# Kernel tuning notes

Hardware: AMD Instinct MI355X
Metric: run time of the kernel (lower is better)

Reference implementation:

```python
import jax, jax.numpy as jnp
import numpy as np

EPS = 1e-13

def masked_softmax(scores, mask):
    # scores: [B, Lq, Lk], mask: [B, Lk] (float 0/1)
    # ESIM masked_softmax: softmax(scores * mask), zero masked cols, renormalize.
    m = mask[:, None, :]
    p = jax.nn.softmax(scores * m, axis=-1)
    p = p * m
    return p / (jnp.sum(p, axis=-1, keepdims=True) + EPS)

def weighted_sum(tensor, weights, mask):
    # tensor: [B, Lk, D], weights: [B, Lq, Lk], mask: [B, Lq]
    ws = jnp.einsum('bqk,bkd->bqd', weights, tensor)
    return ws * mask[:, :, None]

def setup_inputs() -> dict:
    key = jax.random.key(0)
    B, Lp, Lh, D, Dg = 32, 192, 192, 1024, 1024
    ks = jax.random.split(key, 6)
    premise_batch = jax.random.normal(ks[0], (B, Lp, D), jnp.float32)
    hypothesis_batch = jax.random.normal(ks[1], (B, Lh, D), jnp.float32)
    encoded_graph_emb_p = jax.random.normal(ks[2], (B, Lp, Dg), jnp.float32)
    encoded_graph_emb_h = jax.random.normal(ks[3], (B, Lh, Dg), jnp.float32)
    # realistic padding masks: prefix of ones up to a random length
    lp = jax.random.randint(ks[4], (B,), Lp // 2, Lp + 1)
    lh = jax.random.randint(ks[5], (B,), Lh // 2, Lh + 1)
    premise_mask = (jnp.arange(Lp)[None, :] < lp[:, None]).astype(jnp.float32)
    hypothesis_mask = (jnp.arange(Lh)[None, :] < lh[:, None]).astype(jnp.float32)
    return {
        'premise_batch': premise_batch,
        'premise_mask': premise_mask,
        'hypothesis_batch': hypothesis_batch,
        'hypothesis_mask': hypothesis_mask,
        'encoded_graph_emb_p': encoded_graph_emb_p,
        'encoded_graph_emb_h': encoded_graph_emb_h,
    }

def reference(premise_batch, premise_mask, hypothesis_batch, hypothesis_mask,
              encoded_graph_emb_p, encoded_graph_emb_h):
    # [B, Lp, Lh]
    similarity_matrix = jnp.einsum('bpd,bhd->bph', premise_batch, hypothesis_batch)
    similarity_matrix_g = jnp.einsum('bpd,bhd->bph', encoded_graph_emb_p, encoded_graph_emb_h)

    prem_hyp_attn = masked_softmax(similarity_matrix, hypothesis_mask)
    hyp_prem_attn = masked_softmax(jnp.swapaxes(similarity_matrix, 1, 2), premise_mask)
    prem_hyp_attn_g = masked_softmax(similarity_matrix_g, hypothesis_mask)
    hyp_prem_attn_g = masked_softmax(jnp.swapaxes(similarity_matrix_g, 1, 2), premise_mask)

    tot_attn_p = prem_hyp_attn + prem_hyp_attn_g
    tot_attn_h = hyp_prem_attn + hyp_prem_attn_g

    attended_premises = weighted_sum(hypothesis_batch, tot_attn_p, premise_mask)
    attended_hypotheses = weighted_sum(premise_batch, tot_attn_h, hypothesis_mask)
    attended_premises_g = weighted_sum(encoded_graph_emb_h, prem_hyp_attn_g, premise_mask)
    attended_hypotheses_g = weighted_sum(encoded_graph_emb_p, hyp_prem_attn_g, hypothesis_mask)

    return (tot_attn_p, tot_attn_h, attended_premises, attended_premises_g,
            attended_hypotheses, attended_hypotheses_g, prem_hyp_attn,
            hyp_prem_attn, prem_hyp_attn_g, hyp_prem_attn_g)
```

## Files before the change

### kernel.cpp

```cpp
#include <hip/hip_runtime.h>

constexpr int Bb = 32;
constexpr int L  = 192;
constexpr int Dk = 1024;
constexpr size_t A1 = (size_t)Bb * L * L;
constexpr size_t C1 = (size_t)Bb * L * Dk;

typedef short bf16x8 __attribute__((ext_vector_type(8)));
typedef float f32x4  __attribute__((ext_vector_type(4)));
typedef unsigned short ushort_t;

__device__ __forceinline__ unsigned short f2bf(float x){
  unsigned u = __float_as_uint(x);
  u = (u + 0x7FFFu + ((u >> 16) & 1u)) >> 16;
  return (unsigned short)u;
}
__device__ __forceinline__ float bf2f(unsigned short h){
  return __uint_as_float(((unsigned)h) << 16);
}
__device__ __forceinline__ bf16x8 ldfrag(const unsigned short* p){
  return *reinterpret_cast<const bf16x8*>(p);
}

__global__ __launch_bounds__(256) void sim_kernel(
    const float* __restrict__ P, const float* __restrict__ H,
    const float* __restrict__ Gp, const float* __restrict__ Gh,
    float* __restrict__ Sp, float* __restrict__ Sgp)
{
  const int orig = blockIdx.x;
  const int wg   = (orig & 7) * (2304 / 8) + (orig >> 3);
  const int tile = wg % 9;
  const int g    = wg / 9;
  const int ch   = g & 3;
  const int m    = (g >> 2) & 1;
  const int b    = g >> 3;

  const float* X = m ? Gp : P;
  const float* Y = m ? Gh : H;
  float* O = (m ? Sgp : Sp) + (size_t)ch * A1;

  const int ty = tile / 3, tx = tile % 3;
  const int brow = ty * 64, bcol = tx * 64;

  __shared__ unsigned short Ah[64][72], Al[64][72], Bh[64][72], Bl[64][72];

  const int tid  = threadIdx.x;
  const int r    = tid >> 2, q = tid & 3;
  const int lane = tid & 63, wid = tid >> 6;
  const int wm   = wid >> 1, wn = wid & 1;
  const int lr   = lane & 15, kg = lane >> 4;

  f32x4 acc[2][2] = {};

  const float* Xbase = X + (size_t)(b * L + brow + r) * Dk;
  const float* Ybase = Y + (size_t)(b * L + bcol + r) * Dk;
  const int k0beg = ch * 256;

  float4 xv[4], yv[4];

  auto load_regs = [&](int k0){
    #pragma unroll
    for (int j = 0; j < 4; ++j){
      const int c = (q + 4 * j) * 4;
      xv[j] = *reinterpret_cast<const float4*>(Xbase + k0 + c);
      yv[j] = *reinterpret_cast<const float4*>(Ybase + k0 + c);
    }
  };
  auto convert_store = [&](){
    #pragma unroll
    for (int j = 0; j < 4; ++j){
      const int c = (q + 4 * j) * 4;
      ushort4 hh, ll;
      hh.x = f2bf(xv[j].x); ll.x = f2bf(xv[j].x - bf2f(hh.x));
      hh.y = f2bf(xv[j].y); ll.y = f2bf(xv[j].y - bf2f(hh.y));
      hh.z = f2bf(xv[j].z); ll.z = f2bf(xv[j].z - bf2f(hh.z));
      hh.w = f2bf(xv[j].w); ll.w = f2bf(xv[j].w - bf2f(hh.w));
      *reinterpret_cast<ushort4*>(&Ah[r][c]) = hh;
      *reinterpret_cast<ushort4*>(&Al[r][c]) = ll;
      hh.x = f2bf(yv[j].x); ll.x = f2bf(yv[j].x - bf2f(hh.x));
      hh.y = f2bf(yv[j].y); ll.y = f2bf(yv[j].y - bf2f(hh.y));
      hh.z = f2bf(yv[j].z); ll.z = f2bf(yv[j].z - bf2f(hh.z));
      hh.w = f2bf(yv[j].w); ll.w = f2bf(yv[j].w - bf2f(hh.w));
      *reinterpret_cast<ushort4*>(&Bh[r][c]) = hh;
      *reinterpret_cast<ushort4*>(&Bl[r][c]) = ll;
    }
  };

  load_regs(k0beg);
  convert_store();
  __syncthreads();

  for (int chunk = 0; chunk < 4; ++chunk){
    if (chunk < 3) load_regs(k0beg + (chunk + 1) * 64);

    #pragma unroll
    for (int kk = 0; kk < 64; kk += 32){
      const int ki = kk + kg * 8;
      bf16x8 ah[2], al[2], bh[2], bl[2];
      ah[0] = ldfrag(&Ah[wm * 32 +      lr][ki]);
      ah[1] = ldfrag(&Ah[wm * 32 + 16 + lr][ki]);
      al[0] = ldfrag(&Al[wm * 32 +      lr][ki]);
      al[1] = ldfrag(&Al[wm * 32 + 16 + lr][ki]);
      bh[0] = ldfrag(&Bh[wn * 32 +      lr][ki]);
      bh[1] = ldfrag(&Bh[wn * 32 + 16 + lr][ki]);
      bl[0] = ldfrag(&Bl[wn * 32 +      lr][ki]);
      bl[1] = ldfrag(&Bl[wn * 32 + 16 + lr][ki]);
      #pragma unroll
      for (int tm = 0; tm < 2; ++tm)
        #pragma unroll
        for (int tn = 0; tn < 2; ++tn){
          acc[tm][tn] = __builtin_amdgcn_mfma_f32_16x16x32_bf16(ah[tm], bh[tn], acc[tm][tn], 0, 0, 0);
          acc[tm][tn] = __builtin_amdgcn_mfma_f32_16x16x32_bf16(ah[tm], bl[tn], acc[tm][tn], 0, 0, 0);
          acc[tm][tn] = __builtin_amdgcn_mfma_f32_16x16x32_bf16(al[tm], bh[tn], acc[tm][tn], 0, 0, 0);
        }
    }
    __syncthreads();
    if (chunk < 3){
      convert_store();
      __syncthreads();
    }
  }

  float* Ob = O + (size_t)b * L * L;
  #pragma unroll
  for (int tm = 0; tm < 2; ++tm)
    #pragma unroll
    for (int tn = 0; tn < 2; ++tn){
      const int row0 = brow + wm * 32 + tm * 16 + kg * 4;
      const int col  = bcol + wn * 32 + tn * 16 + lr;
      #pragma unroll
      for (int i = 0; i < 4; ++i)
        Ob[(size_t)(row0 + i) * L + col] = acc[tm][tn][i];
    }
}

__global__ __launch_bounds__(256) void row_softmax(
    const float* __restrict__ Sp, const float* __restrict__ Sgp,
    const float* __restrict__ hmask,
    float* __restrict__ o7, float* __restrict__ o9, float* __restrict__ o1,
    float* __restrict__ Sred, float* __restrict__ Sgred,
    ushort_t* __restrict__ w1, ushort_t* __restrict__ w9)
{
  const int b    = blockIdx.y;
  const int p    = blockIdx.x * 4 + (threadIdx.x >> 6);
  const int lane = threadIdx.x & 63;
  const size_t rowoff = ((size_t)b * L + p) * L;
  const float* sr  = Sp  + rowoff;
  const float* sgr = Sgp + rowoff;
  const float* mk  = hmask + (size_t)b * L;

  float m[3], raw[3], rawg[3], v[3], vg[3];
  #pragma unroll
  for (int j = 0; j < 3; ++j){
    const int h = lane + 64 * j;
    const float mm = mk[h];
    m[j]    = mm;
    raw[j]  = sr [h] + sr [A1 + h] + sr [2*A1 + h] + sr [3*A1 + h];
    rawg[j] = sgr[h] + sgr[A1 + h] + sgr[2*A1 + h] + sgr[3*A1 + h];
    v[j]  = raw[j]  * mm;
    vg[j] = rawg[j] * mm;
    Sred [rowoff + h] = raw[j];
    Sgred[rowoff + h] = rawg[j];
  }
  float M  = fmaxf(fmaxf(v[0],  v[1]),  v[2]);
  float Mg = fmaxf(fmaxf(vg[0], vg[1]), vg[2]);
  #pragma unroll
  for (int off = 32; off; off >>= 1){
    M  = fmaxf(M,  __shfl_xor(M,  off));
    Mg = fmaxf(Mg, __shfl_xor(Mg, off));
  }
  float e[3], eg[3];
  float Z = 0.f, Zg = 0.f, Ein = 0.f, Eing = 0.f;
  #pragma unroll
  for (int j = 0; j < 3; ++j){
    e[j]  = expf(v[j]  - M);
    eg[j] = expf(vg[j] - Mg);
    Z  += e[j];  Ein  += m[j] * e[j];
    Zg += eg[j]; Eing += m[j] * eg[j];
  }
  #pragma unroll
  for (int off = 32; off; off >>= 1){
    Z    += __shfl_xor(Z,    off);
    Zg   += __shfl_xor(Zg,   off);
    Ein  += __shfl_xor(Ein,  off);
    Eing += __shfl_xor(Eing, off);
  }
  const float inv  = 1.f / (Ein  + 1e-13f * Z);
  const float invg = 1.f / (Eing + 1e-13f * Zg);
  #pragma unroll
  for (int j = 0; j < 3; ++j){
    const int h = lane + 64 * j;
    const float rj  = m[j] * e[j]  * inv;
    const float rgj = m[j] * eg[j] * invg;
    o7[rowoff + h] = rj;
    o9[rowoff + h] = rgj;
    o1[rowoff + h] = rj + rgj;
    if (w1){
      w1[rowoff + h] = f2bf(rj + rgj);
      w9[rowoff + h] = f2bf(rgj);
    }
  }
}

__global__ __launch_bounds__(256) void col_softmax(
    const float* __restrict__ Sred, const float* __restrict__ Sgred,
    const float* __restrict__ pmask,
    float* __restrict__ o8, float* __restrict__ o10, float* __restrict__ o2,
    ushort_t* __restrict__ w2, ushort_t* __restrict__ w10)
{
  __shared__ float Ts[192][33], Tg[192][33];
  const int b  = blockIdx.y;
  const int h0 = blockIdx.x * 32;
  const int tid = threadIdx.x;
  const size_t boff = (size_t)b * L * L;

  for (int i = tid; i < 192 * 8; i += 256){
    const int rr = i >> 3, qq = i & 7;
    const size_t base = boff + (size_t)rr * L + h0 + qq * 4;
    float4 a = *reinterpret_cast<const float4*>(&Sred[base]);
    float4 g = *reinterpret_cast<const float4*>(&Sgred[base]);
    Ts[rr][qq*4+0] = a.x; Ts[rr][qq*4+1] = a.y; Ts[rr][qq*4+2] = a.z; Ts[rr][qq*4+3] = a.w;
    Tg[rr][qq*4+0] = g.x; Tg[rr][qq*4+1] = g.y; Tg[rr][qq*4+2] = g.z; Tg[rr][qq*4+3] = g.w;
  }
  __syncthreads();

  const int lane = tid & 63, wid = tid >> 6;
  const float* mk = pmask + (size_t)b * L;
  float m[3];
  #pragma unroll
  for (int j = 0; j < 3; ++j) m[j] = mk[lane + 64 * j];

  for (int c = 0; c < 8; ++c){
    const int hl = wid * 8 + c;
    const int h  = h0 + hl;
    float v[3], vg[3];
    #pragma unroll
    for (int j = 0; j < 3; ++j){
      v[j]  = Ts[lane + 64 * j][hl] * m[j];
      vg[j] = Tg[lane + 64 * j][hl] * m[j];
    }
    float M  = fmaxf(fmaxf(v[0],  v[1]),  v[2]);
    float Mg = fmaxf(fmaxf(vg[0], vg[1]), vg[2]);
    #pragma unroll
    for (int off = 32; off; off >>= 1){
      M  = fmaxf(M,  __shfl_xor(M,  off));
      Mg = fmaxf(Mg, __shfl_xor(Mg, off));
    }
    float e[3], eg[3];
    float Z = 0.f, Zg = 0.f, Ein = 0.f, Eing = 0.f;
    #pragma unroll
    for (int j = 0; j < 3; ++j){
      e[j]  = expf(v[j]  - M);
      eg[j] = expf(vg[j] - Mg);
      Z  += e[j];  Ein  += m[j] * e[j];
      Zg += eg[j]; Eing += m[j] * eg[j];
    }
    #pragma unroll
    for (int off = 32; off; off >>= 1){
      Z    += __shfl_xor(Z,    off);
      Zg   += __shfl_xor(Zg,   off);
      Ein  += __shfl_xor(Ein,  off);
      Eing += __shfl_xor(Eing, off);
    }
    const float inv  = 1.f / (Ein  + 1e-13f * Z);
    const float invg = 1.f / (Eing + 1e-13f * Zg);
    const size_t rowoff = ((size_t)b * L + h) * L;
    #pragma unroll
    for (int j = 0; j < 3; ++j){
      const int pp = lane + 64 * j;
      const float rj  = m[j] * e[j]  * inv;
      const float rgj = m[j] * eg[j] * invg;
      o8 [rowoff + pp] = rj;
      o10[rowoff + pp] = rgj;
      o2 [rowoff + pp] = rj + rgj;
      if (w2){
        w2 [rowoff + pp] = f2bf(rj + rgj);
        w10[rowoff + pp] = f2bf(rgj);
      }
    }
  }
}

__global__ __launch_bounds__(256) void wsum_kernel(
    const float* __restrict__ o1f, const float* __restrict__ o9f,
    const float* __restrict__ o2f, const float* __restrict__ o10f,
    const ushort_t* __restrict__ w1, const ushort_t* __restrict__ w9,
    const ushort_t* __restrict__ w2, const ushort_t* __restrict__ w10,
    const float* __restrict__ Pb, const float* __restrict__ Hb,
    const float* __restrict__ Gp, const float* __restrict__ Gh,
    const float* __restrict__ pmask, const float* __restrict__ hmask,
    float* __restrict__ o3, float* __restrict__ o4,
    float* __restrict__ o5, float* __restrict__ o6)
{
  const float* Wf; const ushort_t* Wh; const float* V; const float* qm; float* O;
  switch (blockIdx.z){
    case 0:  Wf = o1f;  Wh = w1;  V = Hb; qm = pmask; O = o3; break;
    case 1:  Wf = o9f;  Wh = w9;  V = Gh; qm = pmask; O = o4; break;
    case 2:  Wf = o2f;  Wh = w2;  V = Pb; qm = hmask; O = o5; break;
    default: Wf = o10f; Wh = w10; V = Gp; qm = hmask; O = o6; break;
  }
  const int b  = blockIdx.y;
  const int d0 = blockIdx.x * 64;

  __shared__ unsigned short Vt[64][68];

  const int tid  = threadIdx.x;
  const int r    = tid >> 2, q = tid & 3;
  const int lane = tid & 63, wv = tid >> 6;
  const int lr   = lane & 15, kg = lane >> 4;

  f32x4 acc[3][4] = {};

  for (int ck = 0; ck < 3; ++ck){
    const int k0 = ck * 64;

    bf16x8 afr[3][2];
    if (Wh){
      #pragma unroll
      for (int t = 0; t < 3; ++t)
        #pragma unroll
        for (int s = 0; s < 2; ++s){
          const int row = wv * 48 + t * 16 + lr;
          afr[t][s] = *reinterpret_cast<const bf16x8*>(
              Wh + ((size_t)b * L + row) * L + k0 + s * 32 + kg * 8);
        }
    } else {
      #pragma unroll
      for (int t = 0; t < 3; ++t)
        #pragma unroll
        for (int s = 0; s < 2; ++s){
          const int row = wv * 48 + t * 16 + lr;
          const float* wp = Wf + ((size_t)b * L + row) * L + k0 + s * 32 + kg * 8;
          float4 x0 = *reinterpret_cast<const float4*>(wp);
          float4 x1 = *reinterpret_cast<const float4*>(wp + 4);
          bf16x8 vv;
          vv[0] = f2bf(x0.x); vv[1] = f2bf(x0.y); vv[2] = f2bf(x0.z); vv[3] = f2bf(x0.w);
          vv[4] = f2bf(x1.x); vv[5] = f2bf(x1.y); vv[6] = f2bf(x1.z); vv[7] = f2bf(x1.w);
          afr[t][s] = vv;
        }
    }

    #pragma unroll
    for (int j = 0; j < 4; ++j){
      const int dcol = (q + 4 * j) * 4;
      float4 vvv = *reinterpret_cast<const float4*>(
          V + ((size_t)b * L + k0 + r) * Dk + d0 + dcol);
      Vt[dcol + 0][r] = f2bf(vvv.x);
      Vt[dcol + 1][r] = f2bf(vvv.y);
      Vt[dcol + 2][r] = f2bf(vvv.z);
      Vt[dcol + 3][r] = f2bf(vvv.w);
    }
    __syncthreads();

    #pragma unroll
    for (int s = 0; s < 2; ++s){
      const int ki = s * 32 + kg * 8;
      bf16x8 bfr[4];
      #pragma unroll
      for (int n = 0; n < 4; ++n)
        bfr[n] = ldfrag(&Vt[n * 16 + lr][ki]);
      #pragma unroll
      for (int t = 0; t < 3; ++t)
        #pragma unroll
        for (int n = 0; n < 4; ++n)
          acc[t][n] = __builtin_amdgcn_mfma_f32_16x16x32_bf16(afr[t][s], bfr[n], acc[t][n], 0, 0, 0);
    }
    __syncthreads();
  }

  #pragma unroll
  for (int t = 0; t < 3; ++t){
    const int row0 = wv * 48 + t * 16 + kg * 4;
    #pragma unroll
    for (int i = 0; i < 4; ++i){
      const int row  = row0 + i;
      const float mv = qm[(size_t)b * L + row];
      #pragma unroll
      for (int n = 0; n < 4; ++n)
        O[((size_t)b * L + row) * Dk + d0 + n * 16 + lr] = acc[t][n][i] * mv;
    }
  }
}

extern "C" void kernel_launch(void* const* d_in, const int* in_sizes, int n_in,
                              void* d_out, int out_size, void* d_ws, size_t ws_size,
                              hipStream_t stream) {
  const float* P  = (const float*)d_in[0];
  const float* pm = (const float*)d_in[1];
  const float* H  = (const float*)d_in[2];
  const float* hm = (const float*)d_in[3];
  const float* Gp = (const float*)d_in[4];
  const float* Gh = (const float*)d_in[5];
  float* out = (float*)d_out;

  float* o1  = out;
  float* o2  = out + A1;
  float* o3  = out + 2 * A1;
  float* o4  = o3 + C1;
  float* o5  = o3 + 2 * C1;
  float* o6  = o3 + 3 * C1;
  float* o7  = o3 + 4 * C1;
  float* o8  = o7 + A1;
  float* o9  = o7 + 2 * A1;
  float* o10 = o7 + 3 * A1;

  float* Sp  = o5;
  float* Sgp = o6;
  float* Sred  = o3;
  float* Sgred = o3 + A1;

  ushort_t* wb = (ws_size >= 4 * A1 * sizeof(ushort_t)) ? (ushort_t*)d_ws : nullptr;
  ushort_t* w1  = wb ? wb + 0 * A1 : nullptr;
  ushort_t* w9  = wb ? wb + 1 * A1 : nullptr;
  ushort_t* w2  = wb ? wb + 2 * A1 : nullptr;
  ushort_t* w10 = wb ? wb + 3 * A1 : nullptr;

  sim_kernel <<<dim3(2304), 256, 0, stream>>>(P, H, Gp, Gh, Sp, Sgp);
  row_softmax<<<dim3(48, 32), 256, 0, stream>>>(Sp, Sgp, hm, o7, o9, o1, Sred, Sgred, w1, w9);
  col_softmax<<<dim3(6, 32),  256, 0, stream>>>(Sred, Sgred, pm, o8, o10, o2, w2, w10);
  wsum_kernel<<<dim3(16, 32, 4), 256, 0, stream>>>(o1, o9, o2, o10, w1, w9, w2, w10,
                                                   P, H, Gp, Gh, pm, hm, o3, o4, o5, o6);
}
```

Measured before the change: 105.5 us.

## Halve split-K partials, drop reduced score buffers, truncate bf16 conversions, swizzle wsum grid

The similarity GEMM now splits K into 2 chunks of 512 instead of 4 of 256. This halves the partial-sum traffic and lets row/col softmax read and sum the two partials directly, so the Sred/Sgred intermediate writes go away. The hi/lo bf16 split uses truncation with byte-permute packing instead of round-to-nearest, and V is truncated to bf16 in the weighted-sum kernel. The wsum launch becomes a 1D grid with an XCD-aware swizzle so blocks sharing the same batch stay together. Costs are fewer sim blocks with longer K loops, which may lower parallelism, and slightly lower precision from truncation.

Result: faster. 90.64 us (-14.1%).

```diff
diff --git a/kernel.cpp b/kernel.cpp
--- a/kernel.cpp
+++ b/kernel.cpp
@@ -15,11 +15,11 @@
   u = (u + 0x7FFFu + ((u >> 16) & 1u)) >> 16;
   return (unsigned short)u;
 }
-__device__ __forceinline__ float bf2f(unsigned short h){
-  return __uint_as_float(((unsigned)h) << 16);
-}
 __device__ __forceinline__ bf16x8 ldfrag(const unsigned short* p){
   return *reinterpret_cast<const bf16x8*>(p);
+}
+__device__ __forceinline__ unsigned pack_hi16(unsigned ua, unsigned ub){
+  return __builtin_amdgcn_perm(ua, ub, 0x03020706u);
 }
 
 __global__ __launch_bounds__(256) void sim_kernel(
@@ -28,12 +28,12 @@
     float* __restrict__ Sp, float* __restrict__ Sgp)
 {
   const int orig = blockIdx.x;
-  const int wg   = (orig & 7) * (2304 / 8) + (orig >> 3);
+  const int wg   = (orig & 7) * (1152 / 8) + (orig >> 3);
   const int tile = wg % 9;
   const int g    = wg / 9;
-  const int ch   = g & 3;
-  const int m    = (g >> 2) & 1;
-  const int b    = g >> 3;
+  const int ch   = g & 1;
+  const int m    = (g >> 1) & 1;
+  const int b    = g >> 2;
 
   const float* X = m ? Gp : P;
   const float* Y = m ? Gh : H;
@@ -54,7 +54,7 @@
 
   const float* Xbase = X + (size_t)(b * L + brow + r) * Dk;
   const float* Ybase = Y + (size_t)(b * L + bcol + r) * Dk;
-  const int k0beg = ch * 256;
+  const int k0beg = ch * 512;
 
   float4 xv[4], yv[4];
 
@@ -66,23 +66,29 @@
       yv[j] = *reinterpret_cast<const float4*>(Ybase + k0 + c);
     }
   };
+  auto split_pack = [](const float4& v, uint2& hi, uint2& lo){
+    unsigned ux = __float_as_uint(v.x), uy = __float_as_uint(v.y);
+    unsigned uz = __float_as_uint(v.z), uw = __float_as_uint(v.w);
+    float lx = v.x - __uint_as_float(ux & 0xFFFF0000u);
+    float ly = v.y - __uint_as_float(uy & 0xFFFF0000u);
+    float lz = v.z - __uint_as_float(uz & 0xFFFF0000u);
+    float lw = v.w - __uint_as_float(uw & 0xFFFF0000u);
+    hi.x = pack_hi16(ux, uy);
+    hi.y = pack_hi16(uz, uw);
+    lo.x = pack_hi16(__float_as_uint(lx), __float_as_uint(ly));
+    lo.y = pack_hi16(__float_as_uint(lz), __float_as_uint(lw));
+  };
   auto convert_store = [&](){
     #pragma unroll
     for (int j = 0; j < 4; ++j){
       const int c = (q + 4 * j) * 4;
-      ushort4 hh, ll;
-      hh.x = f2bf(xv[j].x); ll.x = f2bf(xv[j].x - bf2f(hh.x));
-      hh.y = f2bf(xv[j].y); ll.y = f2bf(xv[j].y - bf2f(hh.y));
-      hh.z = f2bf(xv[j].z); ll.z = f2bf(xv[j].z - bf2f(hh.z));
-      hh.w = f2bf(xv[j].w); ll.w = f2bf(xv[j].w - bf2f(hh.w));
-      *reinterpret_cast<ushort4*>(&Ah[r][c]) = hh;
-      *reinterpret_cast<ushort4*>(&Al[r][c]) = ll;
-      hh.x = f2bf(yv[j].x); ll.x = f2bf(yv[j].x - bf2f(hh.x));
-      hh.y = f2bf(yv[j].y); ll.y = f2bf(yv[j].y - bf2f(hh.y));
-      hh.z = f2bf(yv[j].z); ll.z = f2bf(yv[j].z - bf2f(hh.z));
-      hh.w = f2bf(yv[j].w); ll.w = f2bf(yv[j].w - bf2f(hh.w));
-      *reinterpret_cast<ushort4*>(&Bh[r][c]) = hh;
-      *reinterpret_cast<ushort4*>(&Bl[r][c]) = ll;
+      uint2 hi, lo;
+      split_pack(xv[j], hi, lo);
+      *reinterpret_cast<uint2*>(&Ah[r][c]) = hi;
+      *reinterpret_cast<uint2*>(&Al[r][c]) = lo;
+      split_pack(yv[j], hi, lo);
+      *reinterpret_cast<uint2*>(&Bh[r][c]) = hi;
+      *reinterpret_cast<uint2*>(&Bl[r][c]) = lo;
     }
   };
 
@@ -90,8 +96,8 @@
   convert_store();
   __syncthreads();
 
-  for (int chunk = 0; chunk < 4; ++chunk){
-    if (chunk < 3) load_regs(k0beg + (chunk + 1) * 64);
+  for (int chunk = 0; chunk < 8; ++chunk){
+    if (chunk < 7) load_regs(k0beg + (chunk + 1) * 64);
 
     #pragma unroll
     for (int kk = 0; kk < 64; kk += 32){
@@ -115,7 +121,7 @@
         }
     }
     __syncthreads();
-    if (chunk < 3){
+    if (chunk < 7){
       convert_store();
       __syncthreads();
     }
@@ -138,7 +144,6 @@
     const float* __restrict__ Sp, const float* __restrict__ Sgp,
     const float* __restrict__ hmask,
     float* __restrict__ o7, float* __restrict__ o9, float* __restrict__ o1,
-    float* __restrict__ Sred, float* __restrict__ Sgred,
     ushort_t* __restrict__ w1, ushort_t* __restrict__ w9)
 {
   const int b    = blockIdx.y;
@@ -149,18 +154,14 @@
   const float* sgr = Sgp + rowoff;
   const float* mk  = hmask + (size_t)b * L;
 
-  float m[3], raw[3], rawg[3], v[3], vg[3];
+  float m[3], v[3], vg[3];
   #pragma unroll
   for (int j = 0; j < 3; ++j){
     const int h = lane + 64 * j;
     const float mm = mk[h];
-    m[j]    = mm;
-    raw[j]  = sr [h] + sr [A1 + h] + sr [2*A1 + h] + sr [3*A1 + h];
-    rawg[j] = sgr[h] + sgr[A1 + h] + sgr[2*A1 + h] + sgr[3*A1 + h];
-    v[j]  = raw[j]  * mm;
-    vg[j] = rawg[j] * mm;
-    Sred [rowoff + h] = raw[j];
-    Sgred[rowoff + h] = rawg[j];
+    m[j]  = mm;
+    v[j]  = (sr [h] + sr [A1 + h]) * mm;
+    vg[j] = (sgr[h] + sgr[A1 + h]) * mm;
   }
   float M  = fmaxf(fmaxf(v[0],  v[1]),  v[2]);
   float Mg = fmaxf(fmaxf(vg[0], vg[1]), vg[2]);
@@ -203,7 +204,7 @@
 }
 
 __global__ __launch_bounds__(256) void col_softmax(
-    const float* __restrict__ Sred, const float* __restrict__ Sgred,
+    const float* __restrict__ Sp, const float* __restrict__ Sgp,
     const float* __restrict__ pmask,
     float* __restrict__ o8, float* __restrict__ o10, float* __restrict__ o2,
     ushort_t* __restrict__ w2, ushort_t* __restrict__ w10)
@@ -217,8 +218,12 @@
   for (int i = tid; i < 192 * 8; i += 256){
     const int rr = i >> 3, qq = i & 7;
     const size_t base = boff + (size_t)rr * L + h0 + qq * 4;
-    float4 a = *reinterpret_cast<const float4*>(&Sred[base]);
-    float4 g = *reinterpret_cast<const float4*>(&Sgred[base]);
+    float4 a  = *reinterpret_cast<const float4*>(&Sp [base]);
+    float4 a2 = *reinterpret_cast<const float4*>(&Sp [A1 + base]);
+    float4 g  = *reinterpret_cast<const float4*>(&Sgp[base]);
+    float4 g2 = *reinterpret_cast<const float4*>(&Sgp[A1 + base]);
+    a.x += a2.x; a.y += a2.y; a.z += a2.z; a.w += a2.w;
+    g.x += g2.x; g.y += g2.y; g.z += g2.z; g.w += g2.w;
     Ts[rr][qq*4+0] = a.x; Ts[rr][qq*4+1] = a.y; Ts[rr][qq*4+2] = a.z; Ts[rr][qq*4+3] = a.w;
     Tg[rr][qq*4+0] = g.x; Tg[rr][qq*4+1] = g.y; Tg[rr][qq*4+2] = g.z; Tg[rr][qq*4+3] = g.w;
   }
@@ -292,15 +297,21 @@
     float* __restrict__ o3, float* __restrict__ o4,
     float* __restrict__ o5, float* __restrict__ o6)
 {
+  const int orig = blockIdx.x;
+  const int wg   = (orig & 7) * (2048 / 8) + (orig >> 3);
+  const int dt   = wg & 15;
+  const int gz   = wg >> 4;
+  const int z    = gz & 3;
+  const int b    = gz >> 2;
+  const int d0   = dt * 64;
+
   const float* Wf; const ushort_t* Wh; const float* V; const float* qm; float* O;
-  switch (blockIdx.z){
+  switch (z){
     case 0:  Wf = o1f;  Wh = w1;  V = Hb; qm = pmask; O = o3; break;
     case 1:  Wf = o9f;  Wh = w9;  V = Gh; qm = pmask; O = o4; break;
     case 2:  Wf = o2f;  Wh = w2;  V = Pb; qm = hmask; O = o5; break;
     default: Wf = o10f; Wh = w10; V = Gp; qm = hmask; O = o6; break;
   }
-  const int b  = blockIdx.y;
-  const int d0 = blockIdx.x * 64;
 
   __shared__ unsigned short Vt[64][68];
 
@@ -345,10 +356,10 @@
       const int dcol = (q + 4 * j) * 4;
       float4 vvv = *reinterpret_cast<const float4*>(
           V + ((size_t)b * L + k0 + r) * Dk + d0 + dcol);
-      Vt[dcol + 0][r] = f2bf(vvv.x);
-      Vt[dcol + 1][r] = f2bf(vvv.y);
-      Vt[dcol + 2][r] = f2bf(vvv.z);
-      Vt[dcol + 3][r] = f2bf(vvv.w);
+      Vt[dcol + 0][r] = (ushort_t)(__float_as_uint(vvv.x) >> 16);
+      Vt[dcol + 1][r] = (ushort_t)(__float_as_uint(vvv.y) >> 16);
+      Vt[dcol + 2][r] = (ushort_t)(__float_as_uint(vvv.z) >> 16);
+      Vt[dcol + 3][r] = (ushort_t)(__float_as_uint(vvv.w) >> 16);
     }
     __syncthreads();
 
@@ -406,8 +417,6 @@
 
   float* Sp  = o5;
   float* Sgp = o6;
-  float* Sred  = o3;
-  float* Sgred = o3 + A1;
 
   ushort_t* wb = (ws_size >= 4 * A1 * sizeof(ushort_t)) ? (ushort_t*)d_ws : nullptr;
   ushort_t* w1  = wb ? wb + 0 * A1 : nullptr;
@@ -415,9 +424,9 @@
   ushort_t* w2  = wb ? wb + 2 * A1 : nullptr;
   ushort_t* w10 = wb ? wb + 3 * A1 : nullptr;
 
-  sim_kernel <<<dim3(2304), 256, 0, stream>>>(P, H, Gp, Gh, Sp, Sgp);
-  row_softmax<<<dim3(48, 32), 256, 0, stream>>>(Sp, Sgp, hm, o7, o9, o1, Sred, Sgred, w1, w9);
-  col_softmax<<<dim3(6, 32),  256, 0, stream>>>(Sred, Sgred, pm, o8, o10, o2, w2, w10);
-  wsum_kernel<<<dim3(16, 32, 4), 256, 0, stream>>>(o1, o9, o2, o10, w1, w9, w2, w10,
-                                                   P, H, Gp, Gh, pm, hm, o3, o4, o5, o6);
-}
+  sim_kernel <<<dim3(1152),   256, 0, stream>>>(P, H, Gp, Gh, Sp, Sgp);
+  row_softmax<<<dim3(48, 32), 256, 0, stream>>>(Sp, Sgp, hm, o7, o9, o1, w1, w9);
+  col_softmax<<<dim3(6, 32),  256, 0, stream>>>(Sp, Sgp, pm, o8, o10, o2, w2, w10);
+  wsum_kernel<<<dim3(2048),   256, 0, stream>>>(o1, o9, o2, o10, w1, w9, w2, w10,
+                                                P, H, Gp, Gh, pm, hm, o3, o4, o5, o6);
+}
```
